# Kernel optimization log

Hardware: AMD Instinct MI355X
Metric: run time of the kernel (lower is better)

The kernel has to match this reference:

```python
import jax, jax.numpy as jnp
import numpy as np

DIM = 4096
N_HEADS = 32
N_KV_HEADS = 8
HEAD_DIM = DIM // N_HEADS  # 128
N_REP = N_HEADS // N_KV_HEADS  # 4
FFN_HIDDEN = 11008
EPS = 1e-6
B, S = 4, 2048


def rms_norm(x, gamma):
    # x: [b, s, d]
    var = jnp.mean(x * x, axis=-1, keepdims=True)
    return gamma * (x * jax.lax.rsqrt(var + EPS))


def apply_rope(x, cos, sin):
    # x: [b, s, h, d]; cos/sin: [s, d/2]. Complex rotation on (even, odd) pairs.
    x2 = x.reshape(*x.shape[:-1], HEAD_DIM // 2, 2)
    x0, x1 = x2[..., 0], x2[..., 1]
    c = cos[None, :, None, :]
    s = sin[None, :, None, :]
    r0 = x0 * c - x1 * s
    r1 = x0 * s + x1 * c
    return jnp.stack([r0, r1], axis=-1).reshape(x.shape)


def setup_inputs() -> dict:
    key = jax.random.key(0)
    ks = jax.random.split(key, 16)
    sc = 0.02
    inp = {
        "x": jax.random.normal(ks[0], (B, S, DIM), dtype=jnp.float32),
        "freqs": jax.random.uniform(ks[1], (S, HEAD_DIM // 2), dtype=jnp.float32) * (2 * np.pi),
        "start_pos": 0,
        "gamma_attn": jnp.ones((DIM,), jnp.float32),
        "gamma_ffn": jnp.ones((DIM,), jnp.float32),
        "wq_w": sc * jax.random.normal(ks[2], (N_HEADS * HEAD_DIM, DIM), jnp.float32),
        "wq_b": jnp.zeros((N_HEADS * HEAD_DIM,), jnp.float32),
        "wk_w": sc * jax.random.normal(ks[3], (N_KV_HEADS * HEAD_DIM, DIM), jnp.float32),
        "wk_b": jnp.zeros((N_KV_HEADS * HEAD_DIM,), jnp.float32),
        "wv_w": sc * jax.random.normal(ks[4], (N_KV_HEADS * HEAD_DIM, DIM), jnp.float32),
        "wv_b": jnp.zeros((N_KV_HEADS * HEAD_DIM,), jnp.float32),
        "wo_w": sc * jax.random.normal(ks[5], (DIM, N_HEADS * HEAD_DIM), jnp.float32),
        "wo_b": jnp.zeros((DIM,), jnp.float32),
        "w1_w": sc * jax.random.normal(ks[6], (FFN_HIDDEN, DIM), jnp.float32),
        "w3_w": sc * jax.random.normal(ks[7], (FFN_HIDDEN, DIM), jnp.float32),
        "w2_w": sc * jax.random.normal(ks[8], (DIM, FFN_HIDDEN), jnp.float32),
    }
    return inp


def reference(x, freqs, start_pos, gamma_attn, gamma_ffn,
              wq_w, wq_b, wk_w, wk_b, wv_w, wv_b, wo_w, wo_b,
              w1_w, w3_w, w2_w):
    cos, sin = jnp.cos(freqs), jnp.sin(freqs)

    # --- attention sublayer ---
    xn = rms_norm(x, gamma_attn)
    xq = (xn @ wq_w.T + wq_b).reshape(B, S, N_HEADS, HEAD_DIM)
    xk = (xn @ wk_w.T + wk_b).reshape(B, S, N_KV_HEADS, HEAD_DIM)
    xv = (xn @ wv_w.T + wv_b).reshape(B, S, N_KV_HEADS, HEAD_DIM)
    xq = apply_rope(xq, cos, sin)
    xk = apply_rope(xk, cos, sin)

    # KV cache: start_pos=0 prefill -> cache slice [0:start_pos+S] == current xk/xv
    keys = jnp.repeat(xk, N_REP, axis=2)   # [b, s, n_heads, d]
    values = jnp.repeat(xv, N_REP, axis=2)

    scores = jnp.einsum('bqhd,bkhd->bhqk', xq, keys) / np.sqrt(HEAD_DIM)
    probs = jax.nn.softmax(scores.astype(jnp.float32), axis=-1).astype(xq.dtype)
    attn = jnp.einsum('bhqk,bkhd->bqhd', probs, values).reshape(B, S, DIM)
    h = x + attn @ wo_w.T + wo_b

    # --- FFN sublayer (LLaMA SwiGLU) ---
    hn = rms_norm(h, gamma_ffn)
    ff = (jax.nn.silu(hn @ w1_w.T) * (hn @ w3_w.T)) @ w2_w.T
    return h + ff
```

## Files before the change

### kernel.cpp

```cpp
#include <hip/hip_runtime.h>
#include <hip/hip_bf16.h>

#define DIM   4096
#define NH    32
#define NKV   8
#define HD    128
#define FFNH  11008
#define BATCH 4
#define SEQ   2048
#define MTOT  (BATCH*SEQ)

using bf16x8_t = __attribute__((ext_vector_type(8))) short;
using f32x4_t  = __attribute__((ext_vector_type(4))) float;

typedef const __attribute__((address_space(1))) unsigned int GlbU32;
typedef __attribute__((address_space(3))) unsigned int LdsU32;

__device__ __forceinline__ unsigned short f2b(float f) {
  union { float f; unsigned int u; } v; v.f = f;
  return (unsigned short)((v.u + 0x7fffu + ((v.u >> 16) & 1u)) >> 16);
}
__device__ __forceinline__ float b2f(unsigned short b) {
  union { unsigned int u; float f; } v; v.u = ((unsigned int)b) << 16;
  return v.f;
}
__device__ __forceinline__ void gll16(const void* g, void* l) {
  __builtin_amdgcn_global_load_lds((GlbU32*)g, (LdsU32*)l, 16, 0, 0);
}

#define VM8  asm volatile("s_waitcnt vmcnt(8)" ::: "memory")
#define VM4M asm volatile("s_waitcnt vmcnt(4)" ::: "memory")
#define VM0  asm volatile("s_waitcnt vmcnt(0)" ::: "memory")

__global__ __launch_bounds__(256)
void cvt_bf16_k(const float* __restrict__ src, unsigned short* __restrict__ dst)
{
  const size_t i = ((size_t)blockIdx.x * 256 + threadIdx.x) * 8;
  const float4 a = *(const float4*)&src[i];
  const float4 b = *(const float4*)&src[i + 4];
  union { int4 v; unsigned short u[8]; } o;
  o.u[0] = f2b(a.x); o.u[1] = f2b(a.y); o.u[2] = f2b(a.z); o.u[3] = f2b(a.w);
  o.u[4] = f2b(b.x); o.u[5] = f2b(b.y); o.u[6] = f2b(b.z); o.u[7] = f2b(b.w);
  *(int4*)&dst[i] = o.v;
}

__global__ __launch_bounds__(256)
void rmsnorm_k(const float* __restrict__ X, const float* __restrict__ gamma,
               unsigned short* __restrict__ Y)
{
  const int row = blockIdx.x, t = threadIdx.x;
  const float* xr = X + (size_t)row * DIM;
  float4 v[4];
  float ss = 0.f;
#pragma unroll
  for (int p = 0; p < 4; ++p) {
    v[p] = *(const float4*)&xr[p * 1024 + t * 4];
    ss += v[p].x*v[p].x + v[p].y*v[p].y + v[p].z*v[p].z + v[p].w*v[p].w;
  }
#pragma unroll
  for (int off = 32; off >= 1; off >>= 1) ss += __shfl_xor(ss, off, 64);
  __shared__ float red[4];
  if ((t & 63) == 0) red[t >> 6] = ss;
  __syncthreads();
  const float tot = red[0] + red[1] + red[2] + red[3];
  const float rn = rsqrtf(tot * (1.f / DIM) + 1e-6f);
  unsigned short* yr = Y + (size_t)row * DIM;
#pragma unroll
  for (int p = 0; p < 4; ++p) {
    const float4 gv = *(const float4*)&gamma[p * 1024 + t * 4];
    short4 o;
    o.x = (short)f2b(v[p].x * gv.x * rn);
    o.y = (short)f2b(v[p].y * gv.y * rn);
    o.z = (short)f2b(v[p].z * gv.z * rn);
    o.w = (short)f2b(v[p].w * gv.w * rn);
    *(short4*)&yr[p * 1024 + t * 4] = o;
  }
}

template<int NHT>
__global__ __launch_bounds__(256)
void rope_k(unsigned short* __restrict__ buf, const float* __restrict__ fr)
{
  const int u = blockIdx.x * 256 + threadIdx.x;
  const int per_row = NHT * 16;
  const int row  = u / per_row;
  const int rem  = u - row * per_row;
  const int head = rem >> 4;
  const int i4   = (rem & 15) << 2;
  const int s    = row & (SEQ - 1);
  unsigned short* p = buf + (size_t)row * (NHT * HD) + head * HD + i4 * 2;
  union { int4 v; unsigned short u16[8]; } d;
  d.v = *(const int4*)p;
  const float4 f = *(const float4*)&fr[s * 64 + i4];
  const float fa[4] = {f.x, f.y, f.z, f.w};
#pragma unroll
  for (int i = 0; i < 4; ++i) {
    float sn, c;
    __sincosf(fa[i], &sn, &c);
    const float x0 = b2f(d.u16[2*i]), x1 = b2f(d.u16[2*i+1]);
    d.u16[2*i]   = f2b(x0 * c - x1 * sn);
    d.u16[2*i+1] = f2b(x0 * sn + x1 * c);
  }
  *(int4*)p = d.v;
}

template<int MODE>
__global__ __launch_bounds__(512)
void gemm256(const unsigned short* __restrict__ A,
             const unsigned short* __restrict__ W,
             const unsigned short* __restrict__ W3p,
             const float* __restrict__ bias,
             const float* res,
             float* outF,
             unsigned short* __restrict__ outH,
             const unsigned short* __restrict__ wkp,
             const unsigned short* __restrict__ wvp,
             const float* __restrict__ bkp,
             const float* __restrict__ bvp,
             unsigned short* __restrict__ okp,
             unsigned short* __restrict__ ovp,
             int K)
{
  __shared__ __align__(16) char smem[131072];
  const int t = threadIdx.x, lane = t & 63, wid = t >> 6;
  const int wr = wid >> 2, wc = wid & 3;
  const int G = gridDim.x, bid = blockIdx.x;
  const int wg = (bid & 7) * (G >> 3) + (bid >> 3);
  const int NBN = G >> 5;
  const int span = NBN << 3;
  const int tmg = wg / span, rr = wg - tmg * span;
  const int tn = rr >> 3, tm = (tmg << 3) + (rr & 7);
  const int m0 = tm << 8;
  const int NSUB = K >> 5;

  const unsigned short *P1, *P2;
  const float* bp = bias;
  unsigned short* oh = outH;
  int nloc = 0, colsN = 4096;
  if constexpr (MODE == 0) {
    const int n0 = tn << 8;
    if (n0 < 4096)      { nloc = n0;        P1 = W   + (size_t)nloc * K; bp = bias; oh = outH; colsN = 4096; }
    else if (n0 < 5120) { nloc = n0 - 4096; P1 = wkp + (size_t)nloc * K; bp = bkp;  oh = okp;  colsN = 1024; }
    else                { nloc = n0 - 5120; P1 = wvp + (size_t)nloc * K; bp = bvp;  oh = ovp;  colsN = 1024; }
    P2 = P1 + (size_t)128 * K;
  } else if constexpr (MODE == 3) {
    const int n0w = tn << 7;
    P1 = W   + (size_t)n0w * K;
    P2 = W3p + (size_t)n0w * K;
    nloc = n0w;
  } else {
    const int n0 = tn << 8;
    P1 = W + (size_t)n0 * K;
    P2 = P1 + (size_t)128 * K;
    nloc = n0;
  }

  const int r0 = t >> 2, gg = t & 3;
  const int gsw = gg ^ ((r0 >> 1) & 3);

  auto stA = [&](int sig) {
    if (sig < NSUB) {
      const int slot = sig & 3;
      gll16(A + (size_t)(m0 + r0) * K + sig * 32 + gsw * 8,
            smem + slot * 16384 + wid * 1024);
      gll16(A + (size_t)(m0 + 128 + r0) * K + sig * 32 + gsw * 8,
            smem + slot * 16384 + 8192 + wid * 1024);
    }
  };
  auto stB = [&](int sig) {
    if (sig < NSUB) {
      const int slot = sig & 3;
      gll16(P1 + (size_t)r0 * K + sig * 32 + gsw * 8,
            smem + 65536 + slot * 16384 + wid * 1024);
      gll16(P2 + (size_t)r0 * K + sig * 32 + gsw * 8,
            smem + 65536 + slot * 16384 + 8192 + wid * 1024);
    }
  };
  auto rdA = [&](int slot, int mo) -> bf16x8_t {
    const int lrow = wr * 128 + mo + (lane & 15);
    const int g = (lane >> 4) ^ ((lrow >> 1) & 3);
    return *(const bf16x8_t*)(smem + slot * 16384 + lrow * 64 + g * 16);
  };
  auto rdB = [&](int slot, int nf) -> bf16x8_t {
    const int brow = wc * 64 + nf * 16 + (lane & 15);
    const int g = (lane >> 4) ^ ((brow >> 1) & 3);
    return *(const bf16x8_t*)(smem + 65536 + slot * 16384 + brow * 64 + g * 16);
  };

  f32x4_t acc[8][4];
#pragma unroll
  for (int i = 0; i < 8; ++i)
#pragma unroll
    for (int j = 0; j < 4; ++j) acc[i][j] = (f32x4_t)0.f;

  stA(0); stB(0); stA(1); stB(1); stA(2); stB(2);
  VM8;
  __builtin_amdgcn_s_barrier();

  for (int p = 0; p < NSUB; ++p) {
    const int slot = p & 3;
    bf16x8_t bfv[4], afv[8];
#pragma unroll
    for (int n = 0; n < 4; ++n) bfv[n] = rdB(slot, n);
#pragma unroll
    for (int m = 0; m < 8; ++m) afv[m] = rdA(slot, m * 16);
    stA(p + 3); stB(p + 3);
    __builtin_amdgcn_s_setprio(1);
#pragma unroll
    for (int m = 0; m < 8; ++m)
#pragma unroll
      for (int n = 0; n < 4; ++n)
        acc[m][n] = __builtin_amdgcn_mfma_f32_16x16x32_bf16(afv[m], bfv[n], acc[m][n], 0, 0, 0);
    __builtin_amdgcn_s_setprio(0);
    if (p < NSUB - 3)      { VM8; }
    else if (p == NSUB - 3){ VM4M; }
    else                   { VM0; }
    __builtin_amdgcn_s_barrier();
  }

  if constexpr (MODE == 0) {
#pragma unroll
    for (int ni = 0; ni < 4; ++ni) {
      const int col = nloc + wc * 64 + ni * 16 + (lane & 15);
      const float bv = bp[col];
#pragma unroll
      for (int mi = 0; mi < 8; ++mi)
#pragma unroll
        for (int r = 0; r < 4; ++r) {
          const int row = m0 + wr * 128 + mi * 16 + (lane >> 4) * 4 + r;
          oh[(size_t)row * colsN + col] = f2b(acc[mi][ni][r] + bv);
        }
    }
  } else if constexpr (MODE == 1 || MODE == 2) {
#pragma unroll
    for (int ni = 0; ni < 4; ++ni) {
      const int col = nloc + wc * 64 + ni * 16 + (lane & 15);
      float bv = 0.f;
      if constexpr (MODE == 1) bv = bias[col];
#pragma unroll
      for (int mi = 0; mi < 8; ++mi)
#pragma unroll
        for (int r = 0; r < 4; ++r) {
          const int row = m0 + wr * 128 + mi * 16 + (lane >> 4) * 4 + r;
          const size_t idx = (size_t)row * 4096 + col;
          outF[idx] = acc[mi][ni][r] + bv + res[idx];
        }
    }
  } else {
    if (wc >= 2) {
      const int widx = wr * 2 + (wc - 2);
#pragma unroll
      for (int ni = 0; ni < 4; ++ni)
#pragma unroll
        for (int mi = 0; mi < 8; ++mi)
#pragma unroll
          for (int r = 0; r < 4; ++r) {
            const int lrow = mi * 16 + (lane >> 4) * 4 + r;
            const int ncol = ni * 16 + (lane & 15);
            *(unsigned short*)(smem + widx * 16384 + lrow * 128 + ncol * 2) =
                f2b(acc[mi][ni][r]);
          }
    }
    __syncthreads();
    if (wc < 2) {
      const int widx = wr * 2 + wc;
#pragma unroll
      for (int ni = 0; ni < 4; ++ni)
#pragma unroll
        for (int mi = 0; mi < 8; ++mi)
#pragma unroll
          for (int r = 0; r < 4; ++r) {
            const int lrow = mi * 16 + (lane >> 4) * 4 + r;
            const int ncol = ni * 16 + (lane & 15);
            const float s3 = b2f(*(const unsigned short*)(smem + widx * 16384 + lrow * 128 + ncol * 2));
            const float s1 = acc[mi][ni][r];
            const float sig = 1.f / (1.f + __expf(-s1));
            const int row = m0 + wr * 128 + lrow;
            outH[(size_t)row * FFNH + nloc + wc * 64 + ncol] = f2b(s1 * sig * s3);
          }
    }
  }
}

__global__ __launch_bounds__(256)
void attn_k(const unsigned short* __restrict__ Q, const unsigned short* __restrict__ Kb,
            const unsigned short* __restrict__ Vb, unsigned short* __restrict__ O)
{
  __shared__ unsigned short Qs[8192];
  __shared__ unsigned short Ks[2][4096];
  __shared__ unsigned short Vt[2][4096];
  __shared__ unsigned short Ps[2][2048];
  const int t = threadIdx.x, lane = t & 63, wid = t >> 6;
  const int bx = blockIdx.x;
  const int qt = bx & 31, h = (bx >> 5) & 31, b = bx >> 10;
  const int kvh = h >> 2;
  const float rs = 0.08838834764831845f;

#pragma unroll
  for (int oo = 0; oo < 4; ++oo) {
    const int o = wid * 4 + oo;
    const int row = o * 4 + (lane >> 4);
    const int gl  = (lane & 15) ^ (row & 7);
    gll16(Q + (size_t)(b * SEQ + qt * 64 + row) * DIM + h * HD + gl * 8, &Qs[o * 512]);
  }

  const unsigned short* Kbase = Kb + (size_t)(b * SEQ) * (NKV * HD) + kvh * HD;
  const unsigned short* Vbase = Vb + (size_t)(b * SEQ) * (NKV * HD) + kvh * HD;

  auto stK = [&](int kt, int slot) {
#pragma unroll
    for (int oo = 0; oo < 2; ++oo) {
      const int o = wid * 2 + oo;
      const int row = o * 4 + (lane >> 4);
      const int gl  = (lane & 15) ^ (row & 7);
      gll16(Kbase + (size_t)(kt * 32 + row) * (NKV * HD) + gl * 8, &Ks[slot][o * 512]);
    }
  };
  const int kv = t >> 3, dc = (t & 7) << 4;
  const int colv = kv ^ ((t & 3) << 3);
  auto ldV = [&](int kt, int4& lo, int4& hi) {
    const unsigned short* gp = Vbase + (size_t)(kt * 32 + kv) * (NKV * HD) + dc;
    lo = *(const int4*)gp;
    hi = *(const int4*)(gp + 8);
  };
  auto wrV = [&](int slot, int4 vlo, int4 vhi) {
    union { int4 v; unsigned short u[8]; } lo, hi;
    lo.v = vlo; hi.v = vhi;
#pragma unroll
    for (int j = 0; j < 8; ++j) Vt[slot][(dc + j) * 32 + colv] = lo.u[j];
#pragma unroll
    for (int j = 0; j < 8; ++j) Vt[slot][(dc + 8 + j) * 32 + colv] = hi.u[j];
  };

  int4 vlo0, vhi0, vlo1, vhi1;
  stK(0, 0); ldV(0, vlo0, vhi0);
  stK(1, 1); ldV(1, vlo1, vhi1);

  f32x4_t oa[8];
#pragma unroll
  for (int i = 0; i < 8; ++i) oa[i] = (f32x4_t)0.f;
  float mrun[4] = {-1e30f, -1e30f, -1e30f, -1e30f};
  float lrun[4] = {0.f, 0.f, 0.f, 0.f};
  const int q0 = wid * 16;

  for (int kp = 0; kp < SEQ / 64; ++kp) {
    VM0;
    wrV(0, vlo0, vhi0);
    wrV(1, vlo1, vhi1);
    asm volatile("s_waitcnt lgkmcnt(0)" ::: "memory");
    __builtin_amdgcn_s_barrier();

    f32x4_t sa0 = (f32x4_t)0.f, sa1 = (f32x4_t)0.f;
    f32x4_t sa2 = (f32x4_t)0.f, sa3 = (f32x4_t)0.f;
    const int arow = q0 + (lane & 15);
    const int kr0 = lane & 15, kr1 = 16 + (lane & 15);
#pragma unroll
    for (int ks = 0; ks < 4; ++ks) {
      const bf16x8_t aq  = *(const bf16x8_t*)&Qs[(arow * 128 + ks * 32 + (lane >> 4) * 8) ^ ((arow & 7) << 3)];
      const bf16x8_t b00 = *(const bf16x8_t*)&Ks[0][(kr0 * 128 + ks * 32 + (lane >> 4) * 8) ^ ((kr0 & 7) << 3)];
      sa0 = __builtin_amdgcn_mfma_f32_16x16x32_bf16(aq, b00, sa0, 0, 0, 0);
      const bf16x8_t b01 = *(const bf16x8_t*)&Ks[0][(kr1 * 128 + ks * 32 + (lane >> 4) * 8) ^ ((kr1 & 7) << 3)];
      sa1 = __builtin_amdgcn_mfma_f32_16x16x32_bf16(aq, b01, sa1, 0, 0, 0);
      const bf16x8_t b10 = *(const bf16x8_t*)&Ks[1][(kr0 * 128 + ks * 32 + (lane >> 4) * 8) ^ ((kr0 & 7) << 3)];
      sa2 = __builtin_amdgcn_mfma_f32_16x16x32_bf16(aq, b10, sa2, 0, 0, 0);
      const bf16x8_t b11 = *(const bf16x8_t*)&Ks[1][(kr1 * 128 + ks * 32 + (lane >> 4) * 8) ^ ((kr1 & 7) << 3)];
      sa3 = __builtin_amdgcn_mfma_f32_16x16x32_bf16(aq, b11, sa3, 0, 0, 0);
    }

    float pm[4];
#pragma unroll
    for (int r = 0; r < 4; ++r) {
      float v = fmaxf(fmaxf(sa0[r], sa1[r]), fmaxf(sa2[r], sa3[r])) * rs;
#pragma unroll
      for (int off = 1; off < 16; off <<= 1) v = fmaxf(v, __shfl_xor(v, off, 64));
      pm[r] = v;
    }
    const int grow = __any(pm[0] > mrun[0] || pm[1] > mrun[1] ||
                           pm[2] > mrun[2] || pm[3] > mrun[3]);
    if (grow) {
#pragma unroll
      for (int r = 0; r < 4; ++r) {
        const float mnew = fmaxf(mrun[r], pm[r]);
        const float corr = __expf(mrun[r] - mnew);
        mrun[r] = mnew;
        lrun[r] *= corr;
#pragma unroll
        for (int i = 0; i < 8; ++i) oa[i][r] *= corr;
      }
    }
    float pv0[4], pv1[4], pv2[4], pv3[4];
#pragma unroll
    for (int r = 0; r < 4; ++r) {
      pv0[r] = __expf(sa0[r] * rs - mrun[r]);
      pv1[r] = __expf(sa1[r] * rs - mrun[r]);
      pv2[r] = __expf(sa2[r] * rs - mrun[r]);
      pv3[r] = __expf(sa3[r] * rs - mrun[r]);
    }
#pragma unroll
    for (int r = 0; r < 4; ++r) {
      float v = pv0[r] + pv1[r] + pv2[r] + pv3[r];
#pragma unroll
      for (int off = 1; off < 16; off <<= 1) v += __shfl_xor(v, off, 64);
      lrun[r] += v;
    }

#pragma unroll
    for (int r = 0; r < 4; ++r) {
      const int prow = (lane >> 4) * 4 + r;
      Ps[0][wid * 512 + prow * 32 + (lane & 15)]      = f2b(pv0[r]);
      Ps[0][wid * 512 + prow * 32 + 16 + (lane & 15)] = f2b(pv1[r]);
      Ps[1][wid * 512 + prow * 32 + (lane & 15)]      = f2b(pv2[r]);
      Ps[1][wid * 512 + prow * 32 + 16 + (lane & 15)] = f2b(pv3[r]);
    }
    const bf16x8_t pf0 = *(const bf16x8_t*)&Ps[0][wid * 512 + (lane & 15) * 32 + (lane >> 4) * 8];
    const bf16x8_t pf1 = *(const bf16x8_t*)&Ps[1][wid * 512 + (lane & 15) * 32 + (lane >> 4) * 8];

#pragma unroll
    for (int nt2 = 0; nt2 < 8; ++nt2) {
      const bf16x8_t vf0 = *(const bf16x8_t*)&Vt[0][(nt2 * 16 + (lane & 15)) * 32 + (((lane >> 4) ^ (nt2 & 3)) << 3)];
      oa[nt2] = __builtin_amdgcn_mfma_f32_16x16x32_bf16(pf0, vf0, oa[nt2], 0, 0, 0);
      const bf16x8_t vf1 = *(const bf16x8_t*)&Vt[1][(nt2 * 16 + (lane & 15)) * 32 + (((lane >> 4) ^ (nt2 & 3)) << 3)];
      oa[nt2] = __builtin_amdgcn_mfma_f32_16x16x32_bf16(pf1, vf1, oa[nt2], 0, 0, 0);
    }
    __builtin_amdgcn_s_barrier();
    if (kp + 1 < SEQ / 64) {
      stK(2 * kp + 2, 0); ldV(2 * kp + 2, vlo0, vhi0);
      stK(2 * kp + 3, 1); ldV(2 * kp + 3, vlo1, vhi1);
    }
  }

  float inv[4];
#pragma unroll
  for (int r = 0; r < 4; ++r) inv[r] = 1.f / lrun[r];
#pragma unroll
  for (int nt2 = 0; nt2 < 8; ++nt2) {
    const int col = h * HD + nt2 * 16 + (lane & 15);
#pragma unroll
    for (int r = 0; r < 4; ++r) {
      const int row = qt * 64 + q0 + (lane >> 4) * 4 + r;
      O[(size_t)(b * SEQ + row) * DIM + col] = f2b(oa[nt2][r] * inv[r]);
    }
  }
}

extern "C" void kernel_launch(void* const* d_in, const int* in_sizes, int n_in,
                              void* d_out, int out_size, void* d_ws, size_t ws_size,
                              hipStream_t stream)
{
  (void)in_sizes; (void)n_in; (void)out_size; (void)ws_size;
  const float* x   = (const float*)d_in[0];
  const float* fr  = (const float*)d_in[1];
  const float* ga  = (const float*)d_in[3];
  const float* gf  = (const float*)d_in[4];
  const float* wq  = (const float*)d_in[5];
  const float* wqb = (const float*)d_in[6];
  const float* wk  = (const float*)d_in[7];
  const float* wkb = (const float*)d_in[8];
  const float* wv  = (const float*)d_in[9];
  const float* wvb = (const float*)d_in[10];
  const float* wo  = (const float*)d_in[11];
  const float* wob = (const float*)d_in[12];
  const float* w1  = (const float*)d_in[13];
  const float* w3  = (const float*)d_in[14];
  const float* w2  = (const float*)d_in[15];
  float* out = (float*)d_out;

  constexpr size_t MB = 1ull << 20;
  char* ws = (char*)d_ws;
  unsigned short* xn = (unsigned short*)(ws);
  unsigned short* qb = (unsigned short*)(ws + 64*MB);
  unsigned short* kb = (unsigned short*)(ws + 128*MB);
  unsigned short* vb = (unsigned short*)(ws + 144*MB);
  unsigned short* ao = (unsigned short*)(ws + 160*MB);
  unsigned short* hn = (unsigned short*)(ws + 224*MB);
  unsigned short* g  = (unsigned short*)(ws);
  unsigned short* wscr = (unsigned short*)(ws + 288*MB);
  unsigned short* wqB = wscr;
  unsigned short* wkB = wscr + 16*MB;
  unsigned short* wvB = wscr + 20*MB;
  unsigned short* woB = wscr;
  unsigned short* w1B = wscr;
  unsigned short* w3B = wscr + 45*MB;
  unsigned short* w2B = wscr;

  rmsnorm_k<<<MTOT, 256, 0, stream>>>(x, ga, xn);
  cvt_bf16_k<<<(NH*HD*DIM)/2048,  256, 0, stream>>>(wq, wqB);
  cvt_bf16_k<<<(NKV*HD*DIM)/2048, 256, 0, stream>>>(wk, wkB);
  cvt_bf16_k<<<(NKV*HD*DIM)/2048, 256, 0, stream>>>(wv, wvB);
  gemm256<0><<<(MTOT/256)*((DIM+2*NKV*HD)/256), 512, 0, stream>>>(
      xn, wqB, nullptr, wqb, nullptr, nullptr, qb,
      wkB, wvB, wkb, wvb, kb, vb, DIM);
  rope_k<NH><<<(MTOT*NH*16)/256,  256, 0, stream>>>(qb, fr);
  rope_k<NKV><<<(MTOT*NKV*16)/256,256, 0, stream>>>(kb, fr);
  attn_k<<<BATCH*NH*(SEQ/64), 256, 0, stream>>>(qb, kb, vb, ao);
  cvt_bf16_k<<<(DIM*DIM)/2048, 256, 0, stream>>>(wo, woB);
  gemm256<1><<<(MTOT/256)*(DIM/256), 512, 0, stream>>>(
      ao, woB, nullptr, wob, x, out, nullptr,
      nullptr, nullptr, nullptr, nullptr, nullptr, nullptr, DIM);
  rmsnorm_k<<<MTOT, 256, 0, stream>>>(out, gf, hn);
  cvt_bf16_k<<<(FFNH*DIM)/2048, 256, 0, stream>>>(w1, w1B);
  cvt_bf16_k<<<(FFNH*DIM)/2048, 256, 0, stream>>>(w3, w3B);
  gemm256<3><<<(MTOT/256)*(FFNH/128), 512, 0, stream>>>(
      hn, w1B, w3B, nullptr, nullptr, nullptr, g,
      nullptr, nullptr, nullptr, nullptr, nullptr, nullptr, DIM);
  cvt_bf16_k<<<(FFNH*DIM)/2048, 256, 0, stream>>>(w2, w2B);
  gemm256<2><<<(MTOT/256)*(DIM/256), 512, 0, stream>>>(
      g, w2B, nullptr, nullptr, out, out, nullptr,
      nullptr, nullptr, nullptr, nullptr, nullptr, nullptr, FFNH);
}
```

Measured before the change: 3.821 ms.

## Double-buffer GEMM register fragments and interleave LDS reads with MFMAs

Restructures the GEMM main loop into a two-step unrolled pipeline. The A/B fragments for the next k-slab are read from LDS into a second register set while MFMAs on the current set run, and the A reads are interleaved between MFMA groups. The global-load wait threshold is tightened from vmcnt(8) to vmcnt(4) to match the new prefetch schedule. It also wraps the attention kernel's QK and PV MFMA blocks in s_setprio raises. The costs are more register pressure from the doubled fragment sets and a trickier wait/barrier schedule at the loop tail.

```diff
diff --git a/kernel.cpp b/kernel.cpp
--- a/kernel.cpp
+++ b/kernel.cpp
@@ -28,7 +28,6 @@
   __builtin_amdgcn_global_load_lds((GlbU32*)g, (LdsU32*)l, 16, 0, 0);
 }
 
-#define VM8  asm volatile("s_waitcnt vmcnt(8)" ::: "memory")
 #define VM4M asm volatile("s_waitcnt vmcnt(4)" ::: "memory")
 #define VM0  asm volatile("s_waitcnt vmcnt(0)" ::: "memory")
 
@@ -193,28 +192,57 @@
 #pragma unroll
     for (int j = 0; j < 4; ++j) acc[i][j] = (f32x4_t)0.f;
 
+  bf16x8_t a[8], b0[4], b1[4];
+
   stA(0); stB(0); stA(1); stB(1); stA(2); stB(2);
-  VM8;
+  VM4M;
   __builtin_amdgcn_s_barrier();
-
-  for (int p = 0; p < NSUB; ++p) {
-    const int slot = p & 3;
-    bf16x8_t bfv[4], afv[8];
-#pragma unroll
-    for (int n = 0; n < 4; ++n) bfv[n] = rdB(slot, n);
-#pragma unroll
-    for (int m = 0; m < 8; ++m) afv[m] = rdA(slot, m * 16);
+#pragma unroll
+  for (int n = 0; n < 4; ++n) b0[n] = rdB(0, n);
+#pragma unroll
+  for (int m = 0; m < 8; ++m) a[m] = rdA(0, m * 16);
+
+  for (int p = 0; p < NSUB; p += 2) {
     stA(p + 3); stB(p + 3);
-    __builtin_amdgcn_s_setprio(1);
-#pragma unroll
-    for (int m = 0; m < 8; ++m)
-#pragma unroll
-      for (int n = 0; n < 4; ++n)
-        acc[m][n] = __builtin_amdgcn_mfma_f32_16x16x32_bf16(afv[m], bfv[n], acc[m][n], 0, 0, 0);
-    __builtin_amdgcn_s_setprio(0);
-    if (p < NSUB - 3)      { VM8; }
-    else if (p == NSUB - 3){ VM4M; }
-    else                   { VM0; }
+    {
+      const int sn = (p + 1) & 3;
+      const bool more = (p + 1 < NSUB);
+      if (more) {
+#pragma unroll
+        for (int n = 0; n < 4; ++n) b1[n] = rdB(sn, n);
+      }
+      __builtin_amdgcn_s_setprio(1);
+#pragma unroll
+      for (int m = 0; m < 8; ++m) {
+#pragma unroll
+        for (int n = 0; n < 4; ++n)
+          acc[m][n] = __builtin_amdgcn_mfma_f32_16x16x32_bf16(a[m], b0[n], acc[m][n], 0, 0, 0);
+        if (more) a[m] = rdA(sn, m * 16);
+      }
+      __builtin_amdgcn_s_setprio(0);
+    }
+    if (p + 3 < NSUB) { VM4M; } else { VM0; }
+    __builtin_amdgcn_s_barrier();
+
+    stA(p + 4); stB(p + 4);
+    {
+      const int sn = (p + 2) & 3;
+      const bool more = (p + 2 < NSUB);
+      if (more) {
+#pragma unroll
+        for (int n = 0; n < 4; ++n) b0[n] = rdB(sn, n);
+      }
+      __builtin_amdgcn_s_setprio(1);
+#pragma unroll
+      for (int m = 0; m < 8; ++m) {
+#pragma unroll
+        for (int n = 0; n < 4; ++n)
+          acc[m][n] = __builtin_amdgcn_mfma_f32_16x16x32_bf16(a[m], b1[n], acc[m][n], 0, 0, 0);
+        if (more) a[m] = rdA(sn, m * 16);
+      }
+      __builtin_amdgcn_s_setprio(0);
+    }
+    if (p + 4 < NSUB) { VM4M; } else { VM0; }
     __builtin_amdgcn_s_barrier();
   }
 
@@ -354,6 +382,7 @@
     f32x4_t sa2 = (f32x4_t)0.f, sa3 = (f32x4_t)0.f;
     const int arow = q0 + (lane & 15);
     const int kr0 = lane & 15, kr1 = 16 + (lane & 15);
+    __builtin_amdgcn_s_setprio(1);
 #pragma unroll
     for (int ks = 0; ks < 4; ++ks) {
       const bf16x8_t aq  = *(const bf16x8_t*)&Qs[(arow * 128 + ks * 32 + (lane >> 4) * 8) ^ ((arow & 7) << 3)];
@@ -366,6 +395,7 @@
       const bf16x8_t b11 = *(const bf16x8_t*)&Ks[1][(kr1 * 128 + ks * 32 + (lane >> 4) * 8) ^ ((kr1 & 7) << 3)];
       sa3 = __builtin_amdgcn_mfma_f32_16x16x32_bf16(aq, b11, sa3, 0, 0, 0);
     }
+    __builtin_amdgcn_s_setprio(0);
 
     float pm[4];
 #pragma unroll
@@ -415,6 +445,7 @@
     const bf16x8_t pf0 = *(const bf16x8_t*)&Ps[0][wid * 512 + (lane & 15) * 32 + (lane >> 4) * 8];
     const bf16x8_t pf1 = *(const bf16x8_t*)&Ps[1][wid * 512 + (lane & 15) * 32 + (lane >> 4) * 8];
 
+    __builtin_amdgcn_s_setprio(1);
 #pragma unroll
     for (int nt2 = 0; nt2 < 8; ++nt2) {
       const bf16x8_t vf0 = *(const bf16x8_t*)&Vt[0][(nt2 * 16 + (lane & 15)) * 32 + (((lane >> 4) ^ (nt2 & 3)) << 3)];
@@ -422,6 +453,7 @@
       const bf16x8_t vf1 = *(const bf16x8_t*)&Vt[1][(nt2 * 16 + (lane & 15)) * 32 + (((lane >> 4) ^ (nt2 & 3)) << 3)];
       oa[nt2] = __builtin_amdgcn_mfma_f32_16x16x32_bf16(pf1, vf1, oa[nt2], 0, 0, 0);
     }
+    __builtin_amdgcn_s_setprio(0);
     __builtin_amdgcn_s_barrier();
     if (kp + 1 < SEQ / 64) {
       stK(2 * kp + 2, 0); ldV(2 * kp + 2, vlo0, vhi0);
```

Measured after the change: 3.861 ms. No clear change (+1.1%).

## Deepen attention K/V prefetch to two pairs ahead and raise MFMA priority

Applied to the files above, without the earlier changes.

The attention kernel now keeps four K tiles in LDS and two sets of V register buffers, so global loads for the next pair of key tiles are issued a full iteration earlier and wait only on the older batch (VM8 instead of VM0). The loop is unrolled by two with alternating buffer sets. s_setprio is raised around the QK and PV MFMA sections so compute waves are favoured. This costs more LDS (an extra 16KB) and more registers, which may lower occupancy.

```diff
diff --git a/kernel.cpp b/kernel.cpp
--- a/kernel.cpp
+++ b/kernel.cpp
@@ -287,7 +287,7 @@
             const unsigned short* __restrict__ Vb, unsigned short* __restrict__ O)
 {
   __shared__ unsigned short Qs[8192];
-  __shared__ unsigned short Ks[2][4096];
+  __shared__ unsigned short Ks[4][4096];
   __shared__ unsigned short Vt[2][4096];
   __shared__ unsigned short Ps[2][2048];
   const int t = threadIdx.x, lane = t & 63, wid = t >> 6;
@@ -295,6 +295,7 @@
   const int qt = bx & 31, h = (bx >> 5) & 31, b = bx >> 10;
   const int kvh = h >> 2;
   const float rs = 0.08838834764831845f;
+  constexpr int NPAIR = SEQ / 64;
 
 #pragma unroll
   for (int oo = 0; oo < 4; ++oo) {
@@ -332,9 +333,9 @@
     for (int j = 0; j < 8; ++j) Vt[slot][(dc + 8 + j) * 32 + colv] = hi.u[j];
   };
 
-  int4 vlo0, vhi0, vlo1, vhi1;
-  stK(0, 0); ldV(0, vlo0, vhi0);
-  stK(1, 1); ldV(1, vlo1, vhi1);
+  int4 a0l, a0h, a1l, a1h, b0l, b0h, b1l, b1h;
+  stK(0, 0); ldV(0, a0l, a0h); stK(1, 1); ldV(1, a1l, a1h);
+  stK(2, 2); ldV(2, b0l, b0h); stK(3, 3); ldV(3, b1l, b1h);
 
   f32x4_t oa[8];
 #pragma unroll
@@ -343,10 +344,10 @@
   float lrun[4] = {0.f, 0.f, 0.f, 0.f};
   const int q0 = wid * 16;
 
-  for (int kp = 0; kp < SEQ / 64; ++kp) {
-    VM0;
-    wrV(0, vlo0, vhi0);
-    wrV(1, vlo1, vhi1);
+  auto pairIter = [&](int p, int sb, int4& l0, int4& h0, int4& l1, int4& h1) {
+    if (p == NPAIR - 1) { VM0; } else { VM8; }
+    wrV(0, l0, h0);
+    wrV(1, l1, h1);
     asm volatile("s_waitcnt lgkmcnt(0)" ::: "memory");
     __builtin_amdgcn_s_barrier();
 
@@ -354,18 +355,20 @@
     f32x4_t sa2 = (f32x4_t)0.f, sa3 = (f32x4_t)0.f;
     const int arow = q0 + (lane & 15);
     const int kr0 = lane & 15, kr1 = 16 + (lane & 15);
+    __builtin_amdgcn_s_setprio(1);
 #pragma unroll
     for (int ks = 0; ks < 4; ++ks) {
       const bf16x8_t aq  = *(const bf16x8_t*)&Qs[(arow * 128 + ks * 32 + (lane >> 4) * 8) ^ ((arow & 7) << 3)];
-      const bf16x8_t b00 = *(const bf16x8_t*)&Ks[0][(kr0 * 128 + ks * 32 + (lane >> 4) * 8) ^ ((kr0 & 7) << 3)];
-      sa0 = __builtin_amdgcn_mfma_f32_16x16x32_bf16(aq, b00, sa0, 0, 0, 0);
-      const bf16x8_t b01 = *(const bf16x8_t*)&Ks[0][(kr1 * 128 + ks * 32 + (lane >> 4) * 8) ^ ((kr1 & 7) << 3)];
-      sa1 = __builtin_amdgcn_mfma_f32_16x16x32_bf16(aq, b01, sa1, 0, 0, 0);
-      const bf16x8_t b10 = *(const bf16x8_t*)&Ks[1][(kr0 * 128 + ks * 32 + (lane >> 4) * 8) ^ ((kr0 & 7) << 3)];
-      sa2 = __builtin_amdgcn_mfma_f32_16x16x32_bf16(aq, b10, sa2, 0, 0, 0);
-      const bf16x8_t b11 = *(const bf16x8_t*)&Ks[1][(kr1 * 128 + ks * 32 + (lane >> 4) * 8) ^ ((kr1 & 7) << 3)];
-      sa3 = __builtin_amdgcn_mfma_f32_16x16x32_bf16(aq, b11, sa3, 0, 0, 0);
-    }
+      const bf16x8_t k00 = *(const bf16x8_t*)&Ks[sb][(kr0 * 128 + ks * 32 + (lane >> 4) * 8) ^ ((kr0 & 7) << 3)];
+      sa0 = __builtin_amdgcn_mfma_f32_16x16x32_bf16(aq, k00, sa0, 0, 0, 0);
+      const bf16x8_t k01 = *(const bf16x8_t*)&Ks[sb][(kr1 * 128 + ks * 32 + (lane >> 4) * 8) ^ ((kr1 & 7) << 3)];
+      sa1 = __builtin_amdgcn_mfma_f32_16x16x32_bf16(aq, k01, sa1, 0, 0, 0);
+      const bf16x8_t k10 = *(const bf16x8_t*)&Ks[sb + 1][(kr0 * 128 + ks * 32 + (lane >> 4) * 8) ^ ((kr0 & 7) << 3)];
+      sa2 = __builtin_amdgcn_mfma_f32_16x16x32_bf16(aq, k10, sa2, 0, 0, 0);
+      const bf16x8_t k11 = *(const bf16x8_t*)&Ks[sb + 1][(kr1 * 128 + ks * 32 + (lane >> 4) * 8) ^ ((kr1 & 7) << 3)];
+      sa3 = __builtin_amdgcn_mfma_f32_16x16x32_bf16(aq, k11, sa3, 0, 0, 0);
+    }
+    __builtin_amdgcn_s_setprio(0);
 
     float pm[4];
 #pragma unroll
@@ -415,6 +418,7 @@
     const bf16x8_t pf0 = *(const bf16x8_t*)&Ps[0][wid * 512 + (lane & 15) * 32 + (lane >> 4) * 8];
     const bf16x8_t pf1 = *(const bf16x8_t*)&Ps[1][wid * 512 + (lane & 15) * 32 + (lane >> 4) * 8];
 
+    __builtin_amdgcn_s_setprio(1);
 #pragma unroll
     for (int nt2 = 0; nt2 < 8; ++nt2) {
       const bf16x8_t vf0 = *(const bf16x8_t*)&Vt[0][(nt2 * 16 + (lane & 15)) * 32 + (((lane >> 4) ^ (nt2 & 3)) << 3)];
@@ -422,11 +426,17 @@
       const bf16x8_t vf1 = *(const bf16x8_t*)&Vt[1][(nt2 * 16 + (lane & 15)) * 32 + (((lane >> 4) ^ (nt2 & 3)) << 3)];
       oa[nt2] = __builtin_amdgcn_mfma_f32_16x16x32_bf16(pf1, vf1, oa[nt2], 0, 0, 0);
     }
+    __builtin_amdgcn_s_setprio(0);
     __builtin_amdgcn_s_barrier();
-    if (kp + 1 < SEQ / 64) {
-      stK(2 * kp + 2, 0); ldV(2 * kp + 2, vlo0, vhi0);
-      stK(2 * kp + 3, 1); ldV(2 * kp + 3, vlo1, vhi1);
-    }
+    if (p + 2 < NPAIR) {
+      stK(2 * p + 4, sb);     ldV(2 * p + 4, l0, h0);
+      stK(2 * p + 5, sb + 1); ldV(2 * p + 5, l1, h1);
+    }
+  };
+
+  for (int j = 0; j < NPAIR / 2; ++j) {
+    pairIter(2 * j,     0, a0l, a0h, a1l, a1h);
+    pairIter(2 * j + 1, 2, b0l, b0h, b1l, b1h);
   }
 
   float inv[4];
```

Result: no change. 3.791 ms (-0.8%).
